# Kernel optimization log

Measured on AMD Instinct MI355X. Metric: run time of the kernel, lower is better.

The kernel has to match this reference:

```python
import jax, jax.numpy as jnp
import numpy as np

B, M, E, K = 8, 256, 128, 16
H, A, R, RMS = 1024, 256, 1024, 512
NEG = -1e25


def setup_inputs() -> dict:
    key = jax.random.key(0)
    ks = jax.random.split(key, 12)
    inp = {
        "mention_reprs": jax.random.normal(ks[0], (B, M, H), jnp.float32),
        "entities": jax.random.randint(ks[1], (B, E, K), 0, M),
        "entity_masks": jax.random.randint(ks[2], (B, E, K), 0, 2, dtype=jnp.int32),
        "relation_memory": jax.random.normal(ks[3], (R, RMS), jnp.float32),
        # GatedMILAttention params
        "Wv": jax.random.normal(ks[4], (A, H), jnp.float32) / np.sqrt(H),
        "bv": jnp.zeros((A,), jnp.float32),
        "Wu": jax.random.normal(ks[5], (A, H), jnp.float32) / np.sqrt(H),
        "bu": jnp.zeros((A,), jnp.float32),
        "Wa": jax.random.normal(ks[6], (1, A), jnp.float32) / np.sqrt(A),
        "ba": jnp.zeros((1,), jnp.float32),
        # relation memory read linear: Linear(RMS, H)
        "Wr": jax.random.normal(ks[7], (H, RMS), jnp.float32) / np.sqrt(RMS),
        "br": jnp.zeros((H,), jnp.float32),
        # output linear: Linear(H + RMS, H)
        "Wo": jax.random.normal(ks[8], (H, H + RMS), jnp.float32) / np.sqrt(H + RMS),
        "bo": jnp.zeros((H,), jnp.float32),
    }
    return inp


def reference(mention_reprs, entities, entity_masks, relation_memory,
              Wv, bv, Wu, bu, Wa, ba, Wr, br, Wo, bo):
    # gather mention clusters: [B, E, K, H]
    clusters = jax.vmap(lambda m, e: m[e])(mention_reprs, entities)
    # gated MIL attention
    aV = jnp.tanh(jnp.einsum('bekh,ah->beka', clusters, Wv) + bv)
    aU = jax.nn.sigmoid(jnp.einsum('bekh,ah->beka', clusters, Wu) + bu)
    logits = jnp.einsum('beka,oa->beko', aV * aU, Wa) + ba  # [B,E,K,1]
    mask = entity_masks[..., None].astype(bool)
    logits = jnp.where(mask, logits, NEG)
    a = jax.nn.softmax(logits, axis=2)
    # weighted pooling over mentions: [B, E, H]
    entity_reprs = jnp.sum(a * clusters, axis=2)
    # relation memory read (memory detached for the read projection)
    s_w = jax.lax.stop_gradient(relation_memory) @ Wr.T + br        # [R, H]
    s = jnp.einsum('beh,rh->ber', entity_reprs, s_w)                # [B, E, R]
    s = jnp.einsum('ber,rm->bem', s, relation_memory)               # [B, E, RMS]
    out = jnp.concatenate([entity_reprs, s], axis=-1) @ Wo.T + bo   # [B, E, H]
    return out  # dropout is identity at inference
```

## Files before the change

### kernel.cpp

```cpp
#include <hip/hip_runtime.h>
#include <cstdint>
#include <cstddef>

#define NEG_ (-1e25f)

typedef __bf16 bf16x8 __attribute__((ext_vector_type(8)));
typedef float  f32x4  __attribute__((ext_vector_type(4)));
typedef short  s16x8  __attribute__((ext_vector_type(8)));
typedef const __attribute__((address_space(1))) void* gas_t;
typedef __attribute__((address_space(3))) void* las_t;

#define MFMA16 __builtin_amdgcn_mfma_f32_16x16x32_bf16

__device__ __forceinline__ short f2bf(float f) {
  union { float f; unsigned u; } v; v.f = f;
  unsigned r = v.u + 0x7fffu + ((v.u >> 16) & 1u);
  return (short)(r >> 16);
}

__device__ __forceinline__ float bf2f(short s) {
  union { unsigned u; float f; } t; t.u = ((unsigned)(unsigned short)s) << 16;
  return t.f;
}

__device__ __forceinline__ s16x8 cvt8(const float* s) {
  bf16x8 r;
  #pragma unroll
  for (int j = 0; j < 8; ++j) r[j] = (__bf16)s[j];
  union { bf16x8 b; s16x8 s; } u; u.b = r; return u.s;
}

__device__ __forceinline__ void gload(const short* g, short* l) {
  __builtin_amdgcn_global_load_lds((gas_t)g, (las_t)l, 16, 0, 0);
}

struct Params {
  const float* ment; const int* ents; const int* msk;
  const float* rm; const float* Wv; const float* bv; const float* Wu;
  const float* bu; const float* Wa; const float* Wr; const float* br;
  const float* Wo; const float* bo; float* out;
  short *Xb, *Wvb, *Wub, *rmb, *Wrb, *Wo2b, *Wo1b, *swTb, *Ub, *Weffb, *erb;
  float *wpart, *cf, *gw2;
};

__global__ __launch_bounds__(256) void k0(Params p) {
  const int g = blockIdx.x * 256 + threadIdx.x;
  #pragma unroll
  for (int it = 0; it < 5; ++it) {
    int u = g + it * 131072;
    long e = (long)u * 8;
    const float* src; short* dst;
    if (u < 262144)      { src = p.ment + e;                     dst = p.Xb + e; }
    else if (u < 294912) { long o = e - 2097152; src = p.Wv + o; dst = p.Wvb + o; }
    else if (u < 327680) { long o = e - 2359296; src = p.Wu + o; dst = p.Wub + o; }
    else if (u < 393216) { long o = e - 2621440; src = p.rm + o; dst = p.rmb + o; }
    else if (u < 458752) { long o = e - 3145728; src = p.Wr + o; dst = p.Wrb + o; }
    else if (u < 524288) { long o = e - 3670016;
                           src = p.Wo + (o >> 9) * 1536 + 1024 + (o & 511);
                           dst = p.Wo2b + o; }
    else                 { long o = e - 4194304;
                           src = p.Wo + (o >> 10) * 1536 + (o & 1023);
                           dst = p.Wo1b + o; }
    float t[8];
    *(float4*)t       = *(const float4*)src;
    *(float4*)(t + 4) = *(const float4*)(src + 4);
    *(s16x8*)dst = cvt8(t);
  }
}

template <int NT, int EPI>
__device__ void g64(const short* __restrict__ A, int lda,
                    const short* __restrict__ B, int ldb,
                    void* __restrict__ C, int ldc, int m0, int n0,
                    const short* __restrict__ w1, const float* __restrict__ e0,
                    const float* __restrict__ e1, const float* __restrict__ e2,
                    short* lds) {
  short* As = lds;
  short* Bs = lds + 16384;
  const int tid = threadIdx.x, wave = tid >> 6, lane = tid & 63;
  const int quad = lane >> 4, l16 = lane & 15;
  const int wm = (wave & 1) * 32, wn = (wave >> 1) * 32;
  const int srow = tid >> 2, scol = (tid & 3) * 8;
  const short* Ag = A + (long)(m0 + srow) * lda + scol;
  const short* Bg = B + (long)(n0 + srow) * ldb + scol;
  const int wb = wave * 512;
  auto issue = [&](int kt) {
    int buf = kt & 7; int ko = kt * 32;
    gload(Ag + ko, As + buf * 2048 + wb);
    gload(Bg + ko, Bs + buf * 2048 + wb);
  };
  f32x4 acc[2][2] = {};
  issue(0); issue(1); issue(2); issue(3); issue(4); issue(5);
  for (int kt = 0; kt < NT; ++kt) {
    int rem = NT - 1 - kt;
    if (rem >= 5)      asm volatile("s_waitcnt vmcnt(10)" ::: "memory");
    else if (rem == 4) asm volatile("s_waitcnt vmcnt(8)" ::: "memory");
    else if (rem == 3) asm volatile("s_waitcnt vmcnt(6)" ::: "memory");
    else if (rem == 2) asm volatile("s_waitcnt vmcnt(4)" ::: "memory");
    else if (rem == 1) asm volatile("s_waitcnt vmcnt(2)" ::: "memory");
    else               asm volatile("s_waitcnt vmcnt(0)" ::: "memory");
    asm volatile("s_barrier" ::: "memory");
    if (kt + 6 < NT) issue(kt + 6);
    const short* as = As + (kt & 7) * 2048;
    const short* bs = Bs + (kt & 7) * 2048;
    bf16x8 a0 = *(const bf16x8*)&as[(wm + l16) * 32 + quad * 8];
    bf16x8 a1 = *(const bf16x8*)&as[(wm + 16 + l16) * 32 + quad * 8];
    bf16x8 b0 = *(const bf16x8*)&bs[(wn + l16) * 32 + quad * 8];
    bf16x8 b1 = *(const bf16x8*)&bs[(wn + 16 + l16) * 32 + quad * 8];
    acc[0][0] = MFMA16(a0, b0, acc[0][0], 0, 0, 0);
    acc[0][1] = MFMA16(a0, b1, acc[0][1], 0, 0, 0);
    acc[1][0] = MFMA16(a1, b0, acc[1][0], 0, 0, 0);
    acc[1][1] = MFMA16(a1, b1, acc[1][1], 0, 0, 0);
  }
  #pragma unroll
  for (int i = 0; i < 2; ++i)
    #pragma unroll
    for (int j = 0; j < 2; ++j) {
      int col = n0 + wn + j * 16 + l16;
      #pragma unroll
      for (int r = 0; r < 4; ++r) {
        int row = m0 + wm + i * 16 + quad * 4 + r;
        float v = acc[i][j][r];
        if constexpr (EPI == 0) {
          ((short*)C)[(long)row * ldc + col] = f2bf(v);
        } else if constexpr (EPI == 1) {
          v += bf2f(w1[(long)row * 1024 + col]);
          ((short*)C)[(long)row * ldc + col] = f2bf(v);
        } else {
          v += e0[col] + e1[row] * e2[col];
          ((float*)C)[(long)row * ldc + col] = v;
        }
      }
    }
}

__device__ void vu_ring(int mi, int ni, const Params& p, short* lds, float* red) {
  short* As  = lds;
  short* Bvs = lds + 6 * 1024;
  short* Bus = lds + 6 * 1024 + 6 * 2048;
  const int tid = threadIdx.x, wave = tid >> 6, lane = tid & 63;
  const int quad = lane >> 4, l16 = lane & 15;
  const int wm = (wave & 1) * 16, wn = (wave >> 1) * 32;
  const int m0 = mi * 32, n0 = ni * 64;
  const int srow = tid >> 2, scol = (tid & 3) * 8;
  const short* Ag  = p.Xb  + (long)(m0 + srow) * 1024 + scol;
  const short* Bvg = p.Wvb + (long)(n0 + srow) * 1024 + scol;
  const short* Bug = p.Wub + (long)(n0 + srow) * 1024 + scol;
  const int wb = wave * 512;
  auto issue = [&](int kt) {
    int buf = kt % 6; int ko = kt * 32;
    if (wave < 2)
      gload(Ag + ko, As + buf * 1024 + wb);
    gload(Bvg + ko, Bvs + buf * 2048 + wb);
    gload(Bug + ko, Bus + buf * 2048 + wb);
  };
  f32x4 accv[2] = {}, accu[2] = {};
  issue(0); issue(1); issue(2); issue(3);
  for (int kt = 0; kt < 32; ++kt) {
    int rem = 31 - kt;
    if (wave < 2) {
      if (rem >= 3)      asm volatile("s_waitcnt vmcnt(9)" ::: "memory");
      else if (rem == 2) asm volatile("s_waitcnt vmcnt(6)" ::: "memory");
      else if (rem == 1) asm volatile("s_waitcnt vmcnt(3)" ::: "memory");
      else               asm volatile("s_waitcnt vmcnt(0)" ::: "memory");
    } else {
      if (rem >= 3)      asm volatile("s_waitcnt vmcnt(6)" ::: "memory");
      else if (rem == 2) asm volatile("s_waitcnt vmcnt(4)" ::: "memory");
      else if (rem == 1) asm volatile("s_waitcnt vmcnt(2)" ::: "memory");
      else               asm volatile("s_waitcnt vmcnt(0)" ::: "memory");
    }
    asm volatile("s_barrier" ::: "memory");
    if (kt + 4 < 32) issue(kt + 4);
    const short* as  = As  + (kt % 6) * 1024;
    const short* bvs = Bvs + (kt % 6) * 2048;
    const short* bus = Bus + (kt % 6) * 2048;
    bf16x8 af = *(const bf16x8*)&as[(wm + l16) * 32 + quad * 8];
    bf16x8 v0 = *(const bf16x8*)&bvs[(wn + l16) * 32 + quad * 8];
    bf16x8 v1 = *(const bf16x8*)&bvs[(wn + 16 + l16) * 32 + quad * 8];
    bf16x8 u0 = *(const bf16x8*)&bus[(wn + l16) * 32 + quad * 8];
    bf16x8 u1 = *(const bf16x8*)&bus[(wn + 16 + l16) * 32 + quad * 8];
    accv[0] = MFMA16(af, v0, accv[0], 0, 0, 0);
    accv[1] = MFMA16(af, v1, accv[1], 0, 0, 0);
    accu[0] = MFMA16(af, u0, accu[0], 0, 0, 0);
    accu[1] = MFMA16(af, u1, accu[1], 0, 0, 0);
  }
  float wsum[4] = {0.f, 0.f, 0.f, 0.f};
  #pragma unroll
  for (int j = 0; j < 2; ++j) {
    int col = n0 + wn + j * 16 + l16;
    float bvc = p.bv[col], buc = p.bu[col], wac = p.Wa[col];
    #pragma unroll
    for (int r = 0; r < 4; ++r) {
      float vv = tanhf(accv[j][r] + bvc);
      float uu = accu[j][r] + buc;
      wsum[r] += (vv / (1.0f + expf(-uu))) * wac;
    }
  }
  #pragma unroll
  for (int r = 0; r < 4; ++r) {
    float s = wsum[r];
    s += __shfl_down(s, 8, 16);
    s += __shfl_down(s, 4, 16);
    s += __shfl_down(s, 2, 16);
    s += __shfl_down(s, 1, 16);
    if (l16 == 0) red[(wave >> 1) * 32 + wm + quad * 4 + r] = s;
  }
  __syncthreads();
  if (tid < 32) p.wpart[ni * 2048 + m0 + tid] = red[tid] + red[32 + tid];
}

__device__ void gw2_wave(int row, const Params& p) {
  const int lane = threadIdx.x & 63;
  const short* u = p.Ub + (long)row * 1024 + lane * 16;
  union { s16x8 s; bf16x8 b; } w0, w1;
  w0.s = *(const s16x8*)u;
  w1.s = *(const s16x8*)(u + 8);
  float s = 0.f;
  #pragma unroll
  for (int j = 0; j < 8; ++j) s += (float)w0.b[j] + (float)w1.b[j];
  #pragma unroll
  for (int off = 32; off > 0; off >>= 1) s += __shfl_down(s, off);
  if (lane == 0) p.gw2[row] = s;
}

__device__ void entity_wave(int be, const Params& p) {
  const int lane = threadIdx.x & 63;
  const int b = be >> 7;
  float a = NEG_; int idx = 0;
  if (lane < 16) {
    idx = p.ents[be * 16 + lane];
    int j = (b << 8) + idx;
    float lw = p.wpart[j] + p.wpart[2048 + j] + p.wpart[4096 + j] + p.wpart[6144 + j];
    a = p.msk[be * 16 + lane] ? lw : NEG_;
  }
  float m = a;
  m = fmaxf(m, __shfl_xor(m, 1, 16));
  m = fmaxf(m, __shfl_xor(m, 2, 16));
  m = fmaxf(m, __shfl_xor(m, 4, 16));
  m = fmaxf(m, __shfl_xor(m, 8, 16));
  float e = expf(a - m);
  float s = e;
  s += __shfl_xor(s, 1, 16);
  s += __shfl_xor(s, 2, 16);
  s += __shfl_xor(s, 4, 16);
  s += __shfl_xor(s, 8, 16);
  float aw = e / s;
  const float* Xr = p.ment + ((long)b << 18);
  const int h0 = lane * 16;
  float acc[16];
  #pragma unroll
  for (int t = 0; t < 16; ++t) acc[t] = 0.f;
  #pragma unroll
  for (int k = 0; k < 16; ++k) {
    float ak = __shfl(aw, k);
    int   ik = __shfl(idx, k);
    const float* xr = Xr + (long)ik * 1024 + h0;
    f32x4 x0 = *(const f32x4*)(xr);
    f32x4 x1 = *(const f32x4*)(xr + 4);
    f32x4 x2 = *(const f32x4*)(xr + 8);
    f32x4 x3 = *(const f32x4*)(xr + 12);
    #pragma unroll
    for (int t = 0; t < 4; ++t) {
      acc[t]      += ak * x0[t];
      acc[4 + t]  += ak * x1[t];
      acc[8 + t]  += ak * x2[t];
      acc[12 + t] += ak * x3[t];
    }
  }
  short* er = p.erb + (long)be * 1024 + h0;
  *(s16x8*)er       = cvt8(acc);
  *(s16x8*)(er + 8) = cvt8(acc + 8);
  float c = 0.f;
  const float* brp = p.br + h0;
  #pragma unroll
  for (int t = 0; t < 16; ++t) c += acc[t] * brp[t];
  #pragma unroll
  for (int off = 32; off > 0; off >>= 1) c += __shfl_down(c, off);
  if (lane == 0) p.cf[be] = c;
}

__global__ __launch_bounds__(256) void k1(Params p) {
  __shared__ short lds[32768];
  __shared__ float red[64];
  const int blk = blockIdx.x;
  if (blk < 256) {
    vu_ring(blk & 63, blk >> 6, p, lds, red);
  } else if (blk < 512) {
    int q = blk - 256;
    g64<16, 0>(p.Wrb, 512, p.rmb, 512, p.swTb, 1024,
               (q >> 4) * 64, (q & 15) * 64, nullptr, nullptr, nullptr, nullptr, lds);
  } else {
    int q = blk - 512;
    g64<16, 0>(p.Wo2b, 512, p.rmb, 512, p.Ub, 1024,
               (q >> 4) * 64, (q & 15) * 64, nullptr, nullptr, nullptr, nullptr, lds);
  }
}

__global__ __launch_bounds__(256) void k2(Params p) {
  __shared__ short lds[32768];
  const int blk = blockIdx.x;
  if (blk < 256) {
    g64<32, 1>(p.Ub, 1024, p.swTb, 1024, p.Weffb, 1024,
               (blk >> 4) * 64, (blk & 15) * 64, p.Wo1b, nullptr, nullptr, nullptr, lds);
  } else {
    int q = blk - 256;
    int wave = threadIdx.x >> 6;
    gw2_wave(q * 4 + wave, p);
    entity_wave(q * 4 + wave, p);
  }
}

__global__ __launch_bounds__(256) void k3(Params p) {
  __shared__ short lds[32768];
  const int blk = blockIdx.x;
  g64<32, 2>(p.erb, 1024, p.Weffb, 1024, p.out, 1024,
             (blk >> 4) * 64, (blk & 15) * 64, nullptr, p.bo, p.cf, p.gw2, lds);
}

extern "C" void kernel_launch(void* const* d_in, const int* in_sizes, int n_in,
                              void* d_out, int out_size, void* d_ws, size_t ws_size,
                              hipStream_t stream) {
  (void)in_sizes; (void)n_in; (void)out_size; (void)ws_size;
  Params p;
  p.ment = (const float*)d_in[0];
  p.ents = (const int*)d_in[1];
  p.msk  = (const int*)d_in[2];
  p.rm   = (const float*)d_in[3];
  p.Wv   = (const float*)d_in[4];
  p.bv   = (const float*)d_in[5];
  p.Wu   = (const float*)d_in[6];
  p.bu   = (const float*)d_in[7];
  p.Wa   = (const float*)d_in[8];
  p.Wr   = (const float*)d_in[10];
  p.br   = (const float*)d_in[11];
  p.Wo   = (const float*)d_in[12];
  p.bo   = (const float*)d_in[13];
  p.out  = (float*)d_out;

  char* w = (char*)d_ws;
  auto alloc = [&](size_t bytes) {
    void* q = (void*)w; w += (bytes + 255) & ~(size_t)255; return q;
  };
  p.Xb    = (short*)alloc((size_t)2048 * 1024 * 2);
  p.Wvb   = (short*)alloc((size_t)256 * 1024 * 2);
  p.Wub   = (short*)alloc((size_t)256 * 1024 * 2);
  p.rmb   = (short*)alloc((size_t)1024 * 512 * 2);
  p.Wrb   = (short*)alloc((size_t)1024 * 512 * 2);
  p.Wo2b  = (short*)alloc((size_t)1024 * 512 * 2);
  p.Wo1b  = (short*)alloc((size_t)1024 * 1024 * 2);
  p.swTb  = (short*)alloc((size_t)1024 * 1024 * 2);
  p.Ub    = (short*)alloc((size_t)1024 * 1024 * 2);
  p.Weffb = (short*)alloc((size_t)1024 * 1024 * 2);
  p.erb   = (short*)alloc((size_t)1024 * 1024 * 2);
  p.wpart = (float*)alloc((size_t)4 * 2048 * 4);
  p.cf    = (float*)alloc((size_t)1024 * 4);
  p.gw2   = (float*)alloc((size_t)1024 * 4);

  k0<<<512, 256, 0, stream>>>(p);
  k1<<<768, 256, 0, stream>>>(p);
  k2<<<512, 256, 0, stream>>>(p);
  k3<<<256, 256, 0, stream>>>(p);
}
```

Before: 135.7 us.

## Move Wo1 bf16 conversion into k1 and pool entities from bf16 mentions

The Wo1 fp32-to-bf16 conversion leaves the serial k0 pass and runs as 64 extra blocks in k1, beside the GEMM and attention blocks. The entity pooling in k2 now reads the bf16 copy of the mention representations instead of the fp32 originals, halving gather bandwidth. It also hoists the shuffles and batches 8 row loads at a time to raise memory-level parallelism. The cost is that entity representations are pooled from bf16-rounded inputs, which slightly lowers precision.

```diff
diff --git a/kernel.cpp b/kernel.cpp
--- a/kernel.cpp
+++ b/kernel.cpp
@@ -46,7 +46,7 @@
 __global__ __launch_bounds__(256) void k0(Params p) {
   const int g = blockIdx.x * 256 + threadIdx.x;
   #pragma unroll
-  for (int it = 0; it < 5; ++it) {
+  for (int it = 0; it < 4; ++it) {
     int u = g + it * 131072;
     long e = (long)u * 8;
     const float* src; short* dst;
@@ -55,12 +55,9 @@
     else if (u < 327680) { long o = e - 2359296; src = p.Wu + o; dst = p.Wub + o; }
     else if (u < 393216) { long o = e - 2621440; src = p.rm + o; dst = p.rmb + o; }
     else if (u < 458752) { long o = e - 3145728; src = p.Wr + o; dst = p.Wrb + o; }
-    else if (u < 524288) { long o = e - 3670016;
+    else                 { long o = e - 3670016;
                            src = p.Wo + (o >> 9) * 1536 + 1024 + (o & 511);
                            dst = p.Wo2b + o; }
-    else                 { long o = e - 4194304;
-                           src = p.Wo + (o >> 10) * 1536 + (o & 1023);
-                           dst = p.Wo1b + o; }
     float t[8];
     *(float4*)t       = *(const float4*)src;
     *(float4*)(t + 4) = *(const float4*)(src + 4);
@@ -245,26 +242,33 @@
   s += __shfl_xor(s, 4, 16);
   s += __shfl_xor(s, 8, 16);
   float aw = e / s;
-  const float* Xr = p.ment + ((long)b << 18);
+  float ak[16]; int ik[16];
+  #pragma unroll
+  for (int k = 0; k < 16; ++k) { ak[k] = __shfl(aw, k); ik[k] = __shfl(idx, k); }
+  const short* Xr = p.Xb + ((long)b << 18);
   const int h0 = lane * 16;
   float acc[16];
   #pragma unroll
   for (int t = 0; t < 16; ++t) acc[t] = 0.f;
   #pragma unroll
-  for (int k = 0; k < 16; ++k) {
-    float ak = __shfl(aw, k);
-    int   ik = __shfl(idx, k);
-    const float* xr = Xr + (long)ik * 1024 + h0;
-    f32x4 x0 = *(const f32x4*)(xr);
-    f32x4 x1 = *(const f32x4*)(xr + 4);
-    f32x4 x2 = *(const f32x4*)(xr + 8);
-    f32x4 x3 = *(const f32x4*)(xr + 12);
-    #pragma unroll
-    for (int t = 0; t < 4; ++t) {
-      acc[t]      += ak * x0[t];
-      acc[4 + t]  += ak * x1[t];
-      acc[8 + t]  += ak * x2[t];
-      acc[12 + t] += ak * x3[t];
+  for (int c = 0; c < 2; ++c) {
+    s16x8 xv[8][2];
+    #pragma unroll
+    for (int k = 0; k < 8; ++k) {
+      const short* xr = Xr + (long)ik[c * 8 + k] * 1024 + h0;
+      xv[k][0] = *(const s16x8*)xr;
+      xv[k][1] = *(const s16x8*)(xr + 8);
+    }
+    #pragma unroll
+    for (int k = 0; k < 8; ++k) {
+      union { s16x8 s; bf16x8 b; } u0, u1;
+      u0.s = xv[k][0]; u1.s = xv[k][1];
+      float akk = ak[c * 8 + k];
+      #pragma unroll
+      for (int t = 0; t < 8; ++t) {
+        acc[t]     += akk * (float)u0.b[t];
+        acc[8 + t] += akk * (float)u1.b[t];
+      }
     }
   }
   short* er = p.erb + (long)be * 1024 + h0;
@@ -289,10 +293,21 @@
     int q = blk - 256;
     g64<16, 0>(p.Wrb, 512, p.rmb, 512, p.swTb, 1024,
                (q >> 4) * 64, (q & 15) * 64, nullptr, nullptr, nullptr, nullptr, lds);
-  } else {
+  } else if (blk < 768) {
     int q = blk - 512;
     g64<16, 0>(p.Wo2b, 512, p.rmb, 512, p.Ub, 1024,
                (q >> 4) * 64, (q & 15) * 64, nullptr, nullptr, nullptr, nullptr, lds);
+  } else {
+    int g = (blk - 768) * 256 + threadIdx.x;
+    #pragma unroll
+    for (int it = 0; it < 8; ++it) {
+      long o = ((long)(g + it * 16384)) * 8;
+      const float* src = p.Wo + (o >> 10) * 1536 + (o & 1023);
+      float t[8];
+      *(float4*)t       = *(const float4*)src;
+      *(float4*)(t + 4) = *(const float4*)(src + 4);
+      *(s16x8*)(p.Wo1b + o) = cvt8(t);
+    }
   }
 }
 
@@ -357,7 +372,7 @@
   p.gw2   = (float*)alloc((size_t)1024 * 4);
 
   k0<<<512, 256, 0, stream>>>(p);
-  k1<<<768, 256, 0, stream>>>(p);
+  k1<<<832, 256, 0, stream>>>(p);
   k2<<<512, 256, 0, stream>>>(p);
   k3<<<256, 256, 0, stream>>>(p);
 }
```

After: 130.8 us, median of 2. 3.7% less time.
